# Kernel tuning notes

Measured on AMD Instinct MI355X. Metric: run time of the kernel, lower is better.

Reference implementation:

```python
import jax, jax.numpy as jnp
import numpy as np

EPS = 1e-12
NEG = -1e30


def setup_inputs() -> dict:
    key = jax.random.key(0)
    ks = jax.random.split(key, 7)
    B, Nq, Lp, H, D = 96, 35, 180, 768, 128
    q_hidden = jax.random.normal(ks[0], (B, Nq, H), dtype=jnp.float32)
    pos_hidden = jax.random.normal(ks[1], (B, Lp, H), dtype=jnp.float32)
    neg_hidden = jax.random.normal(ks[2], (B, Lp, H), dtype=jnp.float32)
    W = jax.random.normal(ks[3], (H, D), dtype=jnp.float32) * 0.02
    b = jax.random.normal(ks[4], (D,), dtype=jnp.float32) * 0.02
    # non-punctuation filter mask; guarantee at least one valid token per passage
    pos_mask = jax.random.bernoulli(ks[5], 0.85, (B, Lp)).at[:, 0].set(True)
    neg_mask = jax.random.bernoulli(ks[6], 0.85, (B, Lp)).at[:, 0].set(True)
    return {"q_hidden": q_hidden, "pos_hidden": pos_hidden, "neg_hidden": neg_hidden,
            "W": W, "b": b, "pos_mask": pos_mask, "neg_mask": neg_mask}


def _vector_representation(h, W, b):
    # Linear projection then F.normalize(x) with torch default dim=1,
    # i.e. normalization over the SEQUENCE axis (faithful to source).
    x = jnp.einsum('blh,hd->bld', h, W) + b
    norm = jnp.maximum(jnp.sqrt(jnp.sum(x * x, axis=1, keepdims=True)), EPS)
    return x / norm


def _late_interaction(q, p, mask):
    # q: [Bq, Nq, D], p: [Bp, Lp, D], mask: [Bp, Lp] (True = keep token)
    sim = jnp.einsum('qnd,pld->qpnl', q, p)          # [Bq, Bp, Nq, Lp]
    sim = jnp.where(mask[None, :, None, :], sim, NEG)
    return jnp.max(sim, axis=-1).sum(axis=-1)        # MaxSim: max over Lp, sum over Nq


def reference(q_hidden, pos_hidden, neg_hidden, W, b, pos_mask, neg_mask):
    q = _vector_representation(q_hidden, W, b)
    pos = _vector_representation(pos_hidden, W, b)
    neg = _vector_representation(neg_hidden, W, b)
    pos_scores = _late_interaction(q, pos, pos_mask)
    neg_scores = _late_interaction(q, neg, neg_mask)
    return jnp.concatenate((pos_scores, neg_scores), axis=1)  # [B, 2B]
```

## Files before the change

kernel.cpp:

```cpp
#include <hip/hip_runtime.h>

typedef __attribute__((ext_vector_type(4))) float f32x4;
typedef __attribute__((ext_vector_type(8))) short s16x8;
typedef __attribute__((ext_vector_type(4))) short s16x4;
typedef __bf16 bf16x4 __attribute__((ext_vector_type(4)));

#define B_   96
#define NQ   35
#define LP   180
#define H_   768
#define D_   128
#define NEGF (-1e30f)

#define NROWS 37920
#define QROWS 3360
#define PROWS 17280

__device__ __forceinline__ unsigned short f2bf(float f) {
    return __builtin_bit_cast(unsigned short, (__bf16)f);
}

__device__ __forceinline__ s16x4 cvt_bf4(f32x4 v) {
    return __builtin_bit_cast(s16x4, __builtin_convertvector(v, bf16x4));
}

__device__ __forceinline__ s16x8 pack_bf16(f32x4 v0, f32x4 v1) {
    bf16x4 h0 = __builtin_convertvector(v0, bf16x4);
    bf16x4 h1 = __builtin_convertvector(v1, bf16x4);
    s16x4 a = __builtin_bit_cast(s16x4, h0), b = __builtin_bit_cast(s16x4, h1);
    return __builtin_shufflevector(a, b, 0, 1, 2, 3, 4, 5, 6, 7);
}

__device__ __forceinline__ void glds16(const void* g, void* l) {
    __builtin_amdgcn_global_load_lds(
        (const __attribute__((address_space(1))) unsigned int*)g,
        (__attribute__((address_space(3))) unsigned int*)l,
        16, 0, 0);
}

__global__ __launch_bounds__(256) void prep_k(
    const float* __restrict__ W, unsigned short* __restrict__ wthi,
    const unsigned int* __restrict__ pmask_w, unsigned int* __restrict__ ctrl,
    float* __restrict__ ssq) {
    __shared__ unsigned int rr[256];
    int b = blockIdx.x, t = threadIdx.x;
    if (b < 48) {
        int tid = b * 256 + t;
        int nt = tid / (24 * 64);
        int r = tid - nt * 24 * 64;
        int ks = r / 64, lane = r - ks * 64;
        int m = lane & 15, quad = lane >> 4;
        unsigned short* o = wthi + (size_t)tid * 8;
#pragma unroll
        for (int j = 0; j < 8; j++) {
            int k = ks * 32 + quad * 8 + j;
            o[j] = f2bf(W[(size_t)k * D_ + nt * 16 + m]);
        }
    } else if (b < 192) {
        ssq[(b - 48) * 256 + t] = 0.f;
    } else {
        unsigned int f1 = 0, f3 = 0, f4 = 0;
        for (int w = t; w < 4320; w += 256) {
            unsigned int v = pmask_w[w];
            f1 |= v & 0x0000ff00u;
            f3 |= v & 0xff000000u;
            if (w & 1) f4 |= v & 0x000000ffu;
        }
        rr[t] = f1; __syncthreads();
        for (int s2 = 128; s2; s2 >>= 1) { if (t < s2) rr[t] |= rr[t + s2]; __syncthreads(); }
        if (!t) ctrl[0] = rr[0];
        __syncthreads();
        rr[t] = f3; __syncthreads();
        for (int s2 = 128; s2; s2 >>= 1) { if (t < s2) rr[t] |= rr[t + s2]; __syncthreads(); }
        if (!t) ctrl[1] = rr[0];
        __syncthreads();
        rr[t] = f4; __syncthreads();
        for (int s2 = 128; s2; s2 >>= 1) { if (t < s2) rr[t] |= rr[t + s2]; __syncthreads(); }
        if (!t) ctrl[2] = rr[0];
    }
}

__global__ __launch_bounds__(256) void proj_k(
    const float* __restrict__ qh, const float* __restrict__ ph, const float* __restrict__ nh,
    const unsigned short* __restrict__ wthi, const float* __restrict__ bias,
    float* __restrict__ x, float* __restrict__ ssq,
    const void* __restrict__ pm, const void* __restrict__ nm,
    const unsigned int* __restrict__ ctrl, unsigned char* __restrict__ maskc) {
    __shared__ unsigned short sh[5120];
    int b = blockIdx.x;
    if (b >= 1185) {
        int i = (b - 1185) * 256 + threadIdx.x;
        const void* src = (i < B_ * LP) ? pm : nm;
        int j = (i < B_ * LP) ? i : i - B_ * LP;
        unsigned int c1 = ctrl[0], c3 = ctrl[1], c4 = ctrl[2];
        bool bit;
        if (c1 > 0)       bit = ((const unsigned char*)src)[j] != 0;
        else if (c3 > 0)  bit = ((const float*)src)[j] != 0.0f;
        else if (c4 > 0)  bit = ((const int*)src)[j] != 0;
        else              bit = ((const long long*)src)[j] != 0;
        maskc[i] = bit ? 1 : 0;
        return;
    }
    int t = threadIdx.x;
    int wave = t >> 6, lane = t & 63;
    const float* src; int row0l; int growbase;
    if (b < 105)      { src = qh; row0l = b * 32;         growbase = row0l; }
    else if (b < 645) { src = ph; row0l = (b - 105) * 32; growbase = QROWS + row0l; }
    else              { src = nh; row0l = (b - 645) * 32; growbase = QROWS + PROWS + row0l; }
    int m = lane & 15, quad = lane >> 4;

    int srow = t >> 4, c = t & 15;
    int sksg = c >> 3, kk = c & 7;
    int woff0 = sksg * 640 + srow * 40 + kk * 4;
    int woff1 = woff0 + 1280;
    int roff = m * 40 + quad * 8;
    const float* gp0 = src + (size_t)(row0l + srow) * H_ + c * 4;
    const float* gp1 = gp0 + (size_t)16 * H_;

    f32x4 acc[2][2];
#pragma unroll
    for (int mt = 0; mt < 2; mt++)
#pragma unroll
        for (int ntl = 0; ntl < 2; ntl++) acc[mt][ntl] = (f32x4){0.f, 0.f, 0.f, 0.f};

    int nt0 = wave * 2, nt1 = wave * 2 + 1;

    f32x4 pv0 = *(const f32x4*)gp0;
    f32x4 pv1 = *(const f32x4*)gp1;

#pragma unroll 2
    for (int s = 0; s < 12; s++) {
        int bufo = (s & 1) * 2560;
        *(s16x4*)&sh[bufo + woff0] = cvt_bf4(pv0);
        *(s16x4*)&sh[bufo + woff1] = cvt_bf4(pv1);
        __syncthreads();
        if (s < 11) {
            pv0 = *(const f32x4*)(gp0 + (s + 1) * 64);
            pv1 = *(const f32x4*)(gp1 + (s + 1) * 64);
        }
#pragma unroll
        for (int ksg = 0; ksg < 2; ksg++) {
            int ksgg = s * 2 + ksg;
            s16x8 a0 = *(const s16x8*)&sh[bufo + ksg * 640 + roff];
            s16x8 a1 = *(const s16x8*)&sh[bufo + ksg * 640 + 1280 + roff];
            s16x8 bh0 = *(const s16x8*)(wthi + ((size_t)(nt0 * 24 + ksgg) * 64 + lane) * 8);
            s16x8 bh1 = *(const s16x8*)(wthi + ((size_t)(nt1 * 24 + ksgg) * 64 + lane) * 8);
            acc[0][0] = __builtin_amdgcn_mfma_f32_16x16x32_bf16(a0, bh0, acc[0][0], 0, 0, 0);
            acc[0][1] = __builtin_amdgcn_mfma_f32_16x16x32_bf16(a0, bh1, acc[0][1], 0, 0, 0);
            acc[1][0] = __builtin_amdgcn_mfma_f32_16x16x32_bf16(a1, bh0, acc[1][0], 0, 0, 0);
            acc[1][1] = __builtin_amdgcn_mfma_f32_16x16x32_bf16(a1, bh1, acc[1][1], 0, 0, 0);
        }
    }

#pragma unroll
    for (int mt = 0; mt < 2; mt++) {
        int base = growbase + mt * 16;
        int bk0, bk1, b1start;
        if (base < QROWS)              { bk0 = base / 35;  bk1 = (base + 15) / 35;
                                         b1start = bk1 * 35; }
        else if (base < QROWS + PROWS) { int r0 = base - QROWS;
                                         bk0 = 96 + r0 / 180;  bk1 = 96 + (r0 + 15) / 180;
                                         b1start = QROWS + (bk1 - 96) * 180; }
        else                           { int r0 = base - QROWS - PROWS;
                                         bk0 = 192 + r0 / 180; bk1 = 192 + (r0 + 15) / 180;
                                         b1start = QROWS + PROWS + (bk1 - 192) * 180; }
#pragma unroll
        for (int ntl = 0; ntl < 2; ntl++) {
            int col = (wave * 2 + ntl) * 16 + m;
            float bv = bias[col];
            f32x4 s4 = acc[mt][ntl];
            float slo = 0.f, shi = 0.f;
#pragma unroll
            for (int r = 0; r < 4; r++) {
                int grow = base + quad * 4 + r;
                float v = s4[r] + bv;
                x[(size_t)grow * D_ + col] = v;
                float v2 = v * v;
                if (bk1 > bk0 && grow >= b1start) shi += v2; else slo += v2;
            }
            slo += __shfl_xor(slo, 16); slo += __shfl_xor(slo, 32);
            if (quad == 0) atomicAdd(ssq + (size_t)bk0 * D_ + col, slo);
            if (bk1 > bk0) {
                shi += __shfl_xor(shi, 16); shi += __shfl_xor(shi, 32);
                if (quad == 0) atomicAdd(ssq + (size_t)bk1 * D_ + col, shi);
            }
        }
    }
}

__global__ __launch_bounds__(256) void scatter_k(
    const float* __restrict__ x, const float* __restrict__ ssq,
    const unsigned char* __restrict__ maskc,
    unsigned short* __restrict__ qfrag, unsigned short* __restrict__ pfrag) {
    int c = blockIdx.x * 256 + threadIdx.x;
    int lane = c & 63, ks = (c >> 6) & 3;
    int quad = lane >> 4, mm = lane & 15;
    int d0 = ks * 32 + quad * 8;
    if (c < 61440) {
        int g = c >> 8;
        int mt = g % 5, qp = g / 5;
        int prow = mt * 16 + mm;
        s16x8 outv = (s16x8){0, 0, 0, 0, 0, 0, 0, 0};
        if (prow < 70) {
            int hi = prow >= 35;
            int bq = qp * 2 + hi;
            int l = prow - hi * 35;
            size_t row = (size_t)bq * 35 + l;
            const f32x4* px = (const f32x4*)(x + row * D_ + d0);
            f32x4 v0 = px[0], v1 = px[1];
            const f32x4* pq = (const f32x4*)(ssq + (size_t)bq * D_ + d0);
            f32x4 q0 = pq[0], q1 = pq[1];
            f32x4 r0, r1;
#pragma unroll
            for (int j = 0; j < 4; j++) {
                r0[j] = rsqrtf(fmaxf(q0[j], 1e-24f));
                r1[j] = rsqrtf(fmaxf(q1[j], 1e-24f));
            }
            outv = pack_bf16(v0 * r0, v1 * r1);
        }
        *(s16x8*)(qfrag + (size_t)c * 8) = outv;
    } else {
        int c2 = c - 61440;
        int g = c2 >> 8;
        int nt = g % 12, pbk = g / 12;
        int l = nt * 16 + mm;
        int lsrc = (l < LP && maskc[pbk * LP + l]) ? l : 0;
        size_t row = QROWS + (size_t)pbk * LP + lsrc;
        const f32x4* px = (const f32x4*)(x + row * D_ + d0);
        f32x4 v0 = px[0], v1 = px[1];
        const f32x4* pq = (const f32x4*)(ssq + (size_t)(96 + pbk) * D_ + d0);
        f32x4 q0 = pq[0], q1 = pq[1];
        f32x4 r0, r1;
#pragma unroll
        for (int j = 0; j < 4; j++) {
            r0[j] = rsqrtf(fmaxf(q0[j], 1e-24f));
            r1[j] = rsqrtf(fmaxf(q1[j], 1e-24f));
        }
        *(s16x8*)(pfrag + (size_t)c2 * 8) = pack_bf16(v0 * r0, v1 * r1);
    }
}

__global__ __launch_bounds__(256, 3) void interact_k(
    const unsigned short* __restrict__ qfrag, const unsigned short* __restrict__ pfrag,
    float* __restrict__ out) {
    __shared__ unsigned short plds[24576];
    int wave = threadIdx.x >> 6, lane = threadIdx.x & 63;
    int b = blockIdx.x;
    int xcd = b & 7, i = b >> 3;
    int c = xcd * 24 + (i % 24);
    int qg = i / 24;
    int side = c / 96, pb = c - side * 96;
    int qp = qg * 4 + wave;
    int m = lane & 15, quad = lane >> 4;

    const unsigned short* pbase = pfrag + (size_t)c * 24576;
    const unsigned short* qbase = qfrag + (size_t)qp * 10240;

#pragma unroll
    for (int ntl = 0; ntl < 3; ntl++) {
        int nt = wave * 3 + ntl;
#pragma unroll
        for (int ks = 0; ks < 4; ks++)
            glds16(pbase + ((size_t)(nt * 4 + ks) * 64 + lane) * 8,
                   &plds[(size_t)(nt * 4 + ks) * 512]);
    }

    s16x8 a[5][4];
#pragma unroll
    for (int mt = 0; mt < 5; mt++)
#pragma unroll
        for (int ks = 0; ks < 4; ks++)
            a[mt][ks] = *(const s16x8*)(qbase + ((size_t)(mt * 4 + ks) * 64 + lane) * 8);

    __syncthreads();

    const f32x4 zero4 = (f32x4){0.f, 0.f, 0.f, 0.f};
    float rmax[5][4];
#pragma unroll
    for (int mt = 0; mt < 5; mt++)
#pragma unroll
        for (int rr = 0; rr < 4; rr++) rmax[mt][rr] = NEGF;

    for (int nt = 0; nt < 12; nt++) {
        s16x8 bfr[4];
#pragma unroll
        for (int ks = 0; ks < 4; ks++)
            bfr[ks] = *(const s16x8*)&plds[((size_t)(nt * 4 + ks) * 64 + lane) * 8];
#pragma unroll
        for (int mt = 0; mt < 5; mt++) {
            f32x4 acc = __builtin_amdgcn_mfma_f32_16x16x32_bf16(a[mt][0], bfr[0], zero4, 0, 0, 0);
            acc = __builtin_amdgcn_mfma_f32_16x16x32_bf16(a[mt][1], bfr[1], acc, 0, 0, 0);
            acc = __builtin_amdgcn_mfma_f32_16x16x32_bf16(a[mt][2], bfr[2], acc, 0, 0, 0);
            acc = __builtin_amdgcn_mfma_f32_16x16x32_bf16(a[mt][3], bfr[3], acc, 0, 0, 0);
#pragma unroll
            for (int rr = 0; rr < 4; rr++)
                rmax[mt][rr] = fmaxf(rmax[mt][rr], acc[rr]);
        }
    }

#pragma unroll
    for (int mt = 0; mt < 5; mt++)
#pragma unroll
        for (int rr = 0; rr < 4; rr++) {
            float v = rmax[mt][rr];
            v = fmaxf(v, __shfl_xor(v, 1));
            v = fmaxf(v, __shfl_xor(v, 2));
            v = fmaxf(v, __shfl_xor(v, 4));
            v = fmaxf(v, __shfl_xor(v, 8));
            rmax[mt][rr] = v;
        }
    float s0 = 0.f, s1 = 0.f;
#pragma unroll
    for (int mt = 0; mt < 5; mt++)
#pragma unroll
        for (int rr = 0; rr < 4; rr++) {
            int prow = mt * 16 + quad * 4 + rr;
            float v = rmax[mt][rr];
            if (prow < 35) s0 += v;
            else if (prow < 70) s1 += v;
        }
    s0 += __shfl_xor(s0, 16); s0 += __shfl_xor(s0, 32);
    s1 += __shfl_xor(s1, 16); s1 += __shfl_xor(s1, 32);
    if (lane == 0) {
        int qb0 = qp * 2, qb1 = qp * 2 + 1;
        out[(size_t)qb0 * (2 * B_) + side * B_ + pb] = s0;
        out[(size_t)qb1 * (2 * B_) + side * B_ + pb] = s1;
    }
}

extern "C" void kernel_launch(void* const* d_in, const int* in_sizes, int n_in,
                              void* d_out, int out_size, void* d_ws, size_t ws_size,
                              hipStream_t stream) {
    const float* qh   = (const float*)d_in[0];
    const float* ph   = (const float*)d_in[1];
    const float* nh   = (const float*)d_in[2];
    const float* W    = (const float*)d_in[3];
    const float* bias = (const float*)d_in[4];
    const void* pmask = d_in[5];
    const void* nmask = d_in[6];
    float* out = (float*)d_out;
    char* ws = (char*)d_ws;

    constexpr size_t CTRL_OFF  = 0;
    constexpr size_t WTHI_OFF  = 256;
    constexpr size_t MASKC_OFF = WTHI_OFF + 196608;
    constexpr size_t SSQ_OFF   = 231424;
    constexpr size_t X_OFF     = SSQ_OFF + 147456;
    constexpr size_t QFRAG_OFF = X_OFF + (size_t)NROWS * D_ * 4;
    constexpr size_t PFRAG_OFF = QFRAG_OFF + 983040;

    unsigned int* ctrl     = (unsigned int*)(ws + CTRL_OFF);
    unsigned short* wthi   = (unsigned short*)(ws + WTHI_OFF);
    unsigned char* maskc   = (unsigned char*)(ws + MASKC_OFF);
    float* ssq             = (float*)(ws + SSQ_OFF);
    float* x               = (float*)(ws + X_OFF);
    unsigned short* qfrag  = (unsigned short*)(ws + QFRAG_OFF);
    unsigned short* pfrag  = (unsigned short*)(ws + PFRAG_OFF);

    prep_k<<<193, 256, 0, stream>>>(W, wthi, (const unsigned int*)pmask, ctrl, ssq);
    proj_k<<<1185 + 135, 256, 0, stream>>>(qh, ph, nh, wthi, bias, x, ssq,
                                           pmask, nmask, ctrl, maskc);
    scatter_k<<<2544, 256, 0, stream>>>(x, ssq, maskc, qfrag, pfrag);
    interact_k<<<2304, 256, 0, stream>>>(qfrag, pfrag, out);
}
```

Baseline: 199.5 us.

## Remove LDS staging in projection; per-wave direct global loads with register double-buffering

The projection kernel no longer stages activations through shared memory with block-wide barriers. Each wave now owns half of a 32-row tile (64 output columns), loads fp32 activations straight from global into registers, converts them to bf16 in registers, and prefetches two k-steps ahead for both A and the pre-swizzled weight fragments. The block count drops by about half, and launch bounds now request three blocks per SM. This removes LDS traffic and __syncthreads stalls and raises MFMA work per wave. In exchange, each activation row is read by two waves with strided per-lane global loads that coalesce less well, and register pressure is higher.

```diff
diff --git a/kernel.cpp b/kernel.cpp
--- a/kernel.cpp
+++ b/kernel.cpp
@@ -80,16 +80,40 @@
     }
 }
 
-__global__ __launch_bounds__(256) void proj_k(
+#define PROJ_BODY(d, sp, PF)                                                              \
+    {                                                                                     \
+        s16x8 a0 = pack_bf16(aq##d[0][0], aq##d[0][1]);                                   \
+        s16x8 a1 = pack_bf16(aq##d[1][0], aq##d[1][1]);                                   \
+        s16x8 b0 = bq##d[0], b1 = bq##d[1], b2 = bq##d[2], b3 = bq##d[3];                 \
+        if (PF) {                                                                         \
+            aq##d[0][0] = *(const f32x4*)(ga0 + (sp) * 32);                               \
+            aq##d[0][1] = *(const f32x4*)(ga0 + (sp) * 32 + 4);                           \
+            aq##d[1][0] = *(const f32x4*)(ga1 + (sp) * 32);                               \
+            aq##d[1][1] = *(const f32x4*)(ga1 + (sp) * 32 + 4);                           \
+            bq##d[0] = wb[(0 * 24 + (sp)) * 64];                                          \
+            bq##d[1] = wb[(1 * 24 + (sp)) * 64];                                          \
+            bq##d[2] = wb[(2 * 24 + (sp)) * 64];                                          \
+            bq##d[3] = wb[(3 * 24 + (sp)) * 64];                                          \
+        }                                                                                 \
+        acc[0][0] = __builtin_amdgcn_mfma_f32_16x16x32_bf16(a0, b0, acc[0][0], 0, 0, 0);  \
+        acc[0][1] = __builtin_amdgcn_mfma_f32_16x16x32_bf16(a0, b1, acc[0][1], 0, 0, 0);  \
+        acc[0][2] = __builtin_amdgcn_mfma_f32_16x16x32_bf16(a0, b2, acc[0][2], 0, 0, 0);  \
+        acc[0][3] = __builtin_amdgcn_mfma_f32_16x16x32_bf16(a0, b3, acc[0][3], 0, 0, 0);  \
+        acc[1][0] = __builtin_amdgcn_mfma_f32_16x16x32_bf16(a1, b0, acc[1][0], 0, 0, 0);  \
+        acc[1][1] = __builtin_amdgcn_mfma_f32_16x16x32_bf16(a1, b1, acc[1][1], 0, 0, 0);  \
+        acc[1][2] = __builtin_amdgcn_mfma_f32_16x16x32_bf16(a1, b2, acc[1][2], 0, 0, 0);  \
+        acc[1][3] = __builtin_amdgcn_mfma_f32_16x16x32_bf16(a1, b3, acc[1][3], 0, 0, 0);  \
+    }
+
+__global__ __launch_bounds__(256, 3) void proj_k(
     const float* __restrict__ qh, const float* __restrict__ ph, const float* __restrict__ nh,
     const unsigned short* __restrict__ wthi, const float* __restrict__ bias,
     float* __restrict__ x, float* __restrict__ ssq,
     const void* __restrict__ pm, const void* __restrict__ nm,
     const unsigned int* __restrict__ ctrl, unsigned char* __restrict__ maskc) {
-    __shared__ unsigned short sh[5120];
     int b = blockIdx.x;
-    if (b >= 1185) {
-        int i = (b - 1185) * 256 + threadIdx.x;
+    if (b >= 593) {
+        int i = (b - 593) * 256 + threadIdx.x;
         const void* src = (i < B_ * LP) ? pm : nm;
         int j = (i < B_ * LP) ? i : i - B_ * LP;
         unsigned int c1 = ctrl[0], c3 = ctrl[1], c4 = ctrl[2];
@@ -103,54 +127,42 @@
     }
     int t = threadIdx.x;
     int wave = t >> 6, lane = t & 63;
+    int w = b * 4 + wave;
+    if (w >= 2370) return;
+    int tile = w >> 1, half = w & 1;
     const float* src; int row0l; int growbase;
-    if (b < 105)      { src = qh; row0l = b * 32;         growbase = row0l; }
-    else if (b < 645) { src = ph; row0l = (b - 105) * 32; growbase = QROWS + row0l; }
-    else              { src = nh; row0l = (b - 645) * 32; growbase = QROWS + PROWS + row0l; }
+    if (tile < 105)      { src = qh; row0l = tile * 32;         growbase = row0l; }
+    else if (tile < 645) { src = ph; row0l = (tile - 105) * 32; growbase = QROWS + row0l; }
+    else                 { src = nh; row0l = (tile - 645) * 32; growbase = QROWS + PROWS + row0l; }
     int m = lane & 15, quad = lane >> 4;
 
-    int srow = t >> 4, c = t & 15;
-    int sksg = c >> 3, kk = c & 7;
-    int woff0 = sksg * 640 + srow * 40 + kk * 4;
-    int woff1 = woff0 + 1280;
-    int roff = m * 40 + quad * 8;
-    const float* gp0 = src + (size_t)(row0l + srow) * H_ + c * 4;
-    const float* gp1 = gp0 + (size_t)16 * H_;
-
-    f32x4 acc[2][2];
+    const float* ga0 = src + (size_t)(row0l + m) * H_ + quad * 8;
+    const float* ga1 = ga0 + (size_t)16 * H_;
+    const s16x8* wb = (const s16x8*)wthi + (size_t)(half * 4) * 24 * 64 + lane;
+
+    f32x4 acc[2][4];
 #pragma unroll
     for (int mt = 0; mt < 2; mt++)
 #pragma unroll
-        for (int ntl = 0; ntl < 2; ntl++) acc[mt][ntl] = (f32x4){0.f, 0.f, 0.f, 0.f};
-
-    int nt0 = wave * 2, nt1 = wave * 2 + 1;
-
-    f32x4 pv0 = *(const f32x4*)gp0;
-    f32x4 pv1 = *(const f32x4*)gp1;
-
-#pragma unroll 2
-    for (int s = 0; s < 12; s++) {
-        int bufo = (s & 1) * 2560;
-        *(s16x4*)&sh[bufo + woff0] = cvt_bf4(pv0);
-        *(s16x4*)&sh[bufo + woff1] = cvt_bf4(pv1);
-        __syncthreads();
-        if (s < 11) {
-            pv0 = *(const f32x4*)(gp0 + (s + 1) * 64);
-            pv1 = *(const f32x4*)(gp1 + (s + 1) * 64);
-        }
-#pragma unroll
-        for (int ksg = 0; ksg < 2; ksg++) {
-            int ksgg = s * 2 + ksg;
-            s16x8 a0 = *(const s16x8*)&sh[bufo + ksg * 640 + roff];
-            s16x8 a1 = *(const s16x8*)&sh[bufo + ksg * 640 + 1280 + roff];
-            s16x8 bh0 = *(const s16x8*)(wthi + ((size_t)(nt0 * 24 + ksgg) * 64 + lane) * 8);
-            s16x8 bh1 = *(const s16x8*)(wthi + ((size_t)(nt1 * 24 + ksgg) * 64 + lane) * 8);
-            acc[0][0] = __builtin_amdgcn_mfma_f32_16x16x32_bf16(a0, bh0, acc[0][0], 0, 0, 0);
-            acc[0][1] = __builtin_amdgcn_mfma_f32_16x16x32_bf16(a0, bh1, acc[0][1], 0, 0, 0);
-            acc[1][0] = __builtin_amdgcn_mfma_f32_16x16x32_bf16(a1, bh0, acc[1][0], 0, 0, 0);
-            acc[1][1] = __builtin_amdgcn_mfma_f32_16x16x32_bf16(a1, bh1, acc[1][1], 0, 0, 0);
-        }
-    }
+        for (int ntl = 0; ntl < 4; ntl++) acc[mt][ntl] = (f32x4){0.f, 0.f, 0.f, 0.f};
+
+    f32x4 aq0[2][2], aq1[2][2];
+    s16x8 bq0[4], bq1[4];
+    aq0[0][0] = *(const f32x4*)(ga0);           aq0[0][1] = *(const f32x4*)(ga0 + 4);
+    aq0[1][0] = *(const f32x4*)(ga1);           aq0[1][1] = *(const f32x4*)(ga1 + 4);
+    bq0[0] = wb[0 * 24 * 64]; bq0[1] = wb[1 * 24 * 64];
+    bq0[2] = wb[2 * 24 * 64]; bq0[3] = wb[3 * 24 * 64];
+    aq1[0][0] = *(const f32x4*)(ga0 + 32);      aq1[0][1] = *(const f32x4*)(ga0 + 36);
+    aq1[1][0] = *(const f32x4*)(ga1 + 32);      aq1[1][1] = *(const f32x4*)(ga1 + 36);
+    bq1[0] = wb[(0 * 24 + 1) * 64]; bq1[1] = wb[(1 * 24 + 1) * 64];
+    bq1[2] = wb[(2 * 24 + 1) * 64]; bq1[3] = wb[(3 * 24 + 1) * 64];
+
+    for (int s = 0; s < 21; s += 2) {
+        PROJ_BODY(0, s + 2, true)
+        PROJ_BODY(1, s + 3, true)
+    }
+    PROJ_BODY(0, 0, false)
+    PROJ_BODY(1, 0, false)
 
 #pragma unroll
     for (int mt = 0; mt < 2; mt++) {
@@ -165,8 +177,8 @@
                                          bk0 = 192 + r0 / 180; bk1 = 192 + (r0 + 15) / 180;
                                          b1start = QROWS + PROWS + (bk1 - 192) * 180; }
 #pragma unroll
-        for (int ntl = 0; ntl < 2; ntl++) {
-            int col = (wave * 2 + ntl) * 16 + m;
+        for (int ntl = 0; ntl < 4; ntl++) {
+            int col = (half * 4 + ntl) * 16 + m;
             float bv = bias[col];
             f32x4 s4 = acc[mt][ntl];
             float slo = 0.f, shi = 0.f;
@@ -358,8 +370,8 @@
     unsigned short* pfrag  = (unsigned short*)(ws + PFRAG_OFF);
 
     prep_k<<<193, 256, 0, stream>>>(W, wthi, (const unsigned int*)pmask, ctrl, ssq);
-    proj_k<<<1185 + 135, 256, 0, stream>>>(qh, ph, nh, wthi, bias, x, ssq,
-                                           pmask, nmask, ctrl, maskc);
+    proj_k<<<593 + 135, 256, 0, stream>>>(qh, ph, nh, wthi, bias, x, ssq,
+                                          pmask, nmask, ctrl, maskc);
     scatter_k<<<2544, 256, 0, stream>>>(x, ssq, maskc, qfrag, pfrag);
     interact_k<<<2304, 256, 0, stream>>>(qfrag, pfrag, out);
 }
```

New measurement: 217.4 us. 1.09x slower.

## Pipeline projection GEMM with async global-to-LDS loads and 4-stage ring buffer

Applied to the files above, without the earlier changes.

Replaces the register-staged, double-buffered fp32-to-bf16 LDS tile load in the projection kernel with direct global_load_lds transfers into a 4-stage swizzled fp32 LDS ring. The kernel converts A to bf16 after reading it from LDS, and prefetches W fragments one stage ahead with inline-asm loads. The loop is fully unrolled with explicit vmcnt waits and barriers. The aim is to hide global-memory latency and remove the per-stage register round-trip. In exchange it uses more LDS (32KB fp32), does the conversion on every LDS read, and relies on hand-tuned wait counts.

```diff
diff --git a/kernel.cpp b/kernel.cpp
--- a/kernel.cpp
+++ b/kernel.cpp
@@ -37,6 +37,23 @@
         (__attribute__((address_space(3))) unsigned int*)l,
         16, 0, 0);
 }
+
+__device__ __forceinline__ s16x8 ldg16(const unsigned short* sbase, unsigned int voff) {
+    s16x8 r;
+    asm volatile("global_load_dwordx4 %0, %1, %2"
+                 : "=v"(r) : "v"(voff), "s"(sbase));
+    return r;
+}
+
+#define WAITV(N) do {                                                 \
+    asm volatile("s_waitcnt vmcnt(" #N ")" ::: "memory");             \
+    __builtin_amdgcn_sched_barrier(0);                                \
+} while (0)
+
+#define BAR() do {                                                    \
+    __builtin_amdgcn_sched_barrier(0);                                \
+    __builtin_amdgcn_s_barrier();                                     \
+} while (0)
 
 __global__ __launch_bounds__(256) void prep_k(
     const float* __restrict__ W, unsigned short* __restrict__ wthi,
@@ -80,13 +97,48 @@
     }
 }
 
-__global__ __launch_bounds__(256) void proj_k(
+#define STAGE(S) do {                                                                     \
+    float* ldw = ld0 + ((S)&3) * 2048;                                                    \
+    glds16(gq0 + (S) * 64, ldw);                                                          \
+    glds16(gq1 + (S) * 64, ldw + 256);                                                    \
+} while (0)
+
+#define LDB(p0, p1, p2, p3, S1) do {                                                      \
+    unsigned int k0 = (unsigned int)((S1) * 2048u);                                       \
+    p0 = ldg16(wthi, ob0 + k0);                                                           \
+    p1 = ldg16(wthi, ob1 + k0);                                                           \
+    p2 = ldg16(wthi, ob0 + k0 + 1024u);                                                   \
+    p3 = ldg16(wthi, ob1 + k0 + 1024u);                                                   \
+} while (0)
+
+#define ACOMP(S, B0, B1, B2, B3) do {                                                     \
+    const float* bb = &lds[((S)&3) * 2048];                                               \
+    f32x4 l, h;                                                                           \
+    l = *(const f32x4*)(bb + rb0 + cA0); h = *(const f32x4*)(bb + rb0 + cA0 + 4);         \
+    s16x8 a00 = pack_bf16(l, h);                                                          \
+    l = *(const f32x4*)(bb + rb1 + cA0); h = *(const f32x4*)(bb + rb1 + cA0 + 4);         \
+    s16x8 a10 = pack_bf16(l, h);                                                          \
+    l = *(const f32x4*)(bb + rb0 + cA1); h = *(const f32x4*)(bb + rb0 + cA1 + 4);         \
+    s16x8 a01 = pack_bf16(l, h);                                                          \
+    l = *(const f32x4*)(bb + rb1 + cA1); h = *(const f32x4*)(bb + rb1 + cA1 + 4);         \
+    s16x8 a11 = pack_bf16(l, h);                                                          \
+    acc[0][0] = __builtin_amdgcn_mfma_f32_16x16x32_bf16(a00, B0, acc[0][0], 0, 0, 0);     \
+    acc[0][1] = __builtin_amdgcn_mfma_f32_16x16x32_bf16(a00, B1, acc[0][1], 0, 0, 0);     \
+    acc[1][0] = __builtin_amdgcn_mfma_f32_16x16x32_bf16(a10, B0, acc[1][0], 0, 0, 0);     \
+    acc[1][1] = __builtin_amdgcn_mfma_f32_16x16x32_bf16(a10, B1, acc[1][1], 0, 0, 0);     \
+    acc[0][0] = __builtin_amdgcn_mfma_f32_16x16x32_bf16(a01, B2, acc[0][0], 0, 0, 0);     \
+    acc[0][1] = __builtin_amdgcn_mfma_f32_16x16x32_bf16(a01, B3, acc[0][1], 0, 0, 0);     \
+    acc[1][0] = __builtin_amdgcn_mfma_f32_16x16x32_bf16(a11, B2, acc[1][0], 0, 0, 0);     \
+    acc[1][1] = __builtin_amdgcn_mfma_f32_16x16x32_bf16(a11, B3, acc[1][1], 0, 0, 0);     \
+} while (0)
+
+__global__ __launch_bounds__(256, 4) void proj_k(
     const float* __restrict__ qh, const float* __restrict__ ph, const float* __restrict__ nh,
     const unsigned short* __restrict__ wthi, const float* __restrict__ bias,
     float* __restrict__ x, float* __restrict__ ssq,
     const void* __restrict__ pm, const void* __restrict__ nm,
     const unsigned int* __restrict__ ctrl, unsigned char* __restrict__ maskc) {
-    __shared__ unsigned short sh[5120];
+    __shared__ float lds[8192];
     int b = blockIdx.x;
     if (b >= 1185) {
         int i = (b - 1185) * 256 + threadIdx.x;
@@ -109,13 +161,22 @@
     else              { src = nh; row0l = (b - 645) * 32; growbase = QROWS + PROWS + row0l; }
     int m = lane & 15, quad = lane >> 4;
 
-    int srow = t >> 4, c = t & 15;
-    int sksg = c >> 3, kk = c & 7;
-    int woff0 = sksg * 640 + srow * 40 + kk * 4;
-    int woff1 = woff0 + 1280;
-    int roff = m * 40 + quad * 8;
-    const float* gp0 = src + (size_t)(row0l + srow) * H_ + c * 4;
-    const float* gp1 = gp0 + (size_t)16 * H_;
+    int r0 = wave * 8 + (lane >> 4);
+    int r1 = r0 + 4;
+    int cg0 = (lane & 15) ^ (2 * (r0 & 7));
+    int cg1 = (lane & 15) ^ (2 * (r1 & 7));
+    const float* gq0 = src + (size_t)(row0l + r0) * H_ + cg0 * 4;
+    const float* gq1 = src + (size_t)(row0l + r1) * H_ + cg1 * 4;
+    float* ld0 = &lds[wave * 512];
+
+    int nt0 = wave * 2, nt1 = wave * 2 + 1;
+    unsigned int ob0 = (unsigned int)(((nt0 * 24) * 64 + lane) * 16);
+    unsigned int ob1 = (unsigned int)(((nt1 * 24) * 64 + lane) * 16);
+
+    int swz = 2 * (m & 7);
+    int rb0 = m * 64, rb1 = (m + 16) * 64;
+    int cA0 = ((quad * 2) ^ swz) * 4;
+    int cA1 = ((8 + quad * 2) ^ swz) * 4;
 
     f32x4 acc[2][2];
 #pragma unroll
@@ -123,34 +184,26 @@
 #pragma unroll
         for (int ntl = 0; ntl < 2; ntl++) acc[mt][ntl] = (f32x4){0.f, 0.f, 0.f, 0.f};
 
-    int nt0 = wave * 2, nt1 = wave * 2 + 1;
-
-    f32x4 pv0 = *(const f32x4*)gp0;
-    f32x4 pv1 = *(const f32x4*)gp1;
-
-#pragma unroll 2
-    for (int s = 0; s < 12; s++) {
-        int bufo = (s & 1) * 2560;
-        *(s16x4*)&sh[bufo + woff0] = cvt_bf4(pv0);
-        *(s16x4*)&sh[bufo + woff1] = cvt_bf4(pv1);
-        __syncthreads();
-        if (s < 11) {
-            pv0 = *(const f32x4*)(gp0 + (s + 1) * 64);
-            pv1 = *(const f32x4*)(gp1 + (s + 1) * 64);
-        }
-#pragma unroll
-        for (int ksg = 0; ksg < 2; ksg++) {
-            int ksgg = s * 2 + ksg;
-            s16x8 a0 = *(const s16x8*)&sh[bufo + ksg * 640 + roff];
-            s16x8 a1 = *(const s16x8*)&sh[bufo + ksg * 640 + 1280 + roff];
-            s16x8 bh0 = *(const s16x8*)(wthi + ((size_t)(nt0 * 24 + ksgg) * 64 + lane) * 8);
-            s16x8 bh1 = *(const s16x8*)(wthi + ((size_t)(nt1 * 24 + ksgg) * 64 + lane) * 8);
-            acc[0][0] = __builtin_amdgcn_mfma_f32_16x16x32_bf16(a0, bh0, acc[0][0], 0, 0, 0);
-            acc[0][1] = __builtin_amdgcn_mfma_f32_16x16x32_bf16(a0, bh1, acc[0][1], 0, 0, 0);
-            acc[1][0] = __builtin_amdgcn_mfma_f32_16x16x32_bf16(a1, bh0, acc[1][0], 0, 0, 0);
-            acc[1][1] = __builtin_amdgcn_mfma_f32_16x16x32_bf16(a1, bh1, acc[1][1], 0, 0, 0);
-        }
-    }
+    s16x8 bA0, bA1, bA2, bA3, bB0, bB1, bB2, bB3;
+
+    STAGE(0);
+    STAGE(1);
+    LDB(bA0, bA1, bA2, bA3, 0);
+    STAGE(2);
+    WAITV(8);
+
+    BAR(); LDB(bB0, bB1, bB2, bB3, 1);  STAGE(3);  WAITV(8); ACOMP(0,  bA0, bA1, bA2, bA3);
+    BAR(); LDB(bA0, bA1, bA2, bA3, 2);  STAGE(4);  WAITV(8); ACOMP(1,  bB0, bB1, bB2, bB3);
+    BAR(); LDB(bB0, bB1, bB2, bB3, 3);  STAGE(5);  WAITV(8); ACOMP(2,  bA0, bA1, bA2, bA3);
+    BAR(); LDB(bA0, bA1, bA2, bA3, 4);  STAGE(6);  WAITV(8); ACOMP(3,  bB0, bB1, bB2, bB3);
+    BAR(); LDB(bB0, bB1, bB2, bB3, 5);  STAGE(7);  WAITV(8); ACOMP(4,  bA0, bA1, bA2, bA3);
+    BAR(); LDB(bA0, bA1, bA2, bA3, 6);  STAGE(8);  WAITV(8); ACOMP(5,  bB0, bB1, bB2, bB3);
+    BAR(); LDB(bB0, bB1, bB2, bB3, 7);  STAGE(9);  WAITV(8); ACOMP(6,  bA0, bA1, bA2, bA3);
+    BAR(); LDB(bA0, bA1, bA2, bA3, 8);  STAGE(10); WAITV(8); ACOMP(7,  bB0, bB1, bB2, bB3);
+    BAR(); LDB(bB0, bB1, bB2, bB3, 9);  STAGE(11); WAITV(8); ACOMP(8,  bA0, bA1, bA2, bA3);
+    BAR(); LDB(bA0, bA1, bA2, bA3, 10);            WAITV(6); ACOMP(9,  bB0, bB1, bB2, bB3);
+    BAR(); LDB(bB0, bB1, bB2, bB3, 11);            WAITV(4); ACOMP(10, bA0, bA1, bA2, bA3);
+    BAR();                                         WAITV(0); ACOMP(11, bB0, bB1, bB2, bB3);
 
 #pragma unroll
     for (int mt = 0; mt < 2; mt++) {
@@ -158,11 +211,11 @@
         int bk0, bk1, b1start;
         if (base < QROWS)              { bk0 = base / 35;  bk1 = (base + 15) / 35;
                                          b1start = bk1 * 35; }
-        else if (base < QROWS + PROWS) { int r0 = base - QROWS;
-                                         bk0 = 96 + r0 / 180;  bk1 = 96 + (r0 + 15) / 180;
+        else if (base < QROWS + PROWS) { int r0e = base - QROWS;
+                                         bk0 = 96 + r0e / 180;  bk1 = 96 + (r0e + 15) / 180;
                                          b1start = QROWS + (bk1 - 96) * 180; }
-        else                           { int r0 = base - QROWS - PROWS;
-                                         bk0 = 192 + r0 / 180; bk1 = 192 + (r0 + 15) / 180;
+        else                           { int r0e = base - QROWS - PROWS;
+                                         bk0 = 192 + r0e / 180; bk1 = 192 + (r0e + 15) / 180;
                                          b1start = QROWS + PROWS + (bk1 - 192) * 180; }
 #pragma unroll
         for (int ntl = 0; ntl < 2; ntl++) {
```

Result: no change. 197.5 us (-1.0%).
